# Kernel tuning notes

Measured on AMD Instinct MI355X. Metric: run time of the kernel, lower is better.

## Reference

```python
import jax, jax.numpy as jnp
import numpy as np

N_HEAD = 16
ROPE_BASE = 10000.0
ROPE_SCALE = 1.0

B, T, C = 4, 2048, 1024


def _rope_cos_sin(seq_len, head_dim, dtype):
    inv_freq = 1.0 / (ROPE_BASE ** (jnp.arange(0, head_dim, 2, dtype=jnp.float32) / head_dim))
    t = jnp.arange(seq_len, dtype=jnp.float32) * ROPE_SCALE
    freqs = jnp.einsum('t,d->td', t, inv_freq)          # [T, D/2]
    emb = jnp.concatenate([freqs, freqs], axis=-1)       # [T, D]
    return jnp.cos(emb).astype(dtype), jnp.sin(emb).astype(dtype)


def _rotate_half(x):
    x1, x2 = jnp.split(x, 2, axis=-1)
    return jnp.concatenate([-x2, x1], axis=-1)


def setup_inputs() -> dict:
    key = jax.random.key(0)
    ks = jax.random.split(key, 5)
    s = 1.0 / np.sqrt(C)  # modest init scale to keep logits sane
    return {
        'x': jax.random.normal(ks[0], (B, T, C), dtype=jnp.float32),
        'wq': jax.random.normal(ks[1], (C, C), dtype=jnp.float32) * s,
        'wk': jax.random.normal(ks[2], (C, C), dtype=jnp.float32) * s,
        'wv': jax.random.normal(ks[3], (C, C), dtype=jnp.float32) * s,
        'wp': jax.random.normal(ks[4], (C, C), dtype=jnp.float32) * s,
    }


def reference(x, wq, wk, wv, wp):
    # x: [B, T, C]; weights are torch Linear layout [out, in] -> y = x @ W.T
    Bx, Tx, Cx = x.shape
    H = N_HEAD
    D = Cx // H
    scale = D ** -0.5

    def split_heads(y):  # [B,T,C] -> [B,H,T,D]
        return y.reshape(Bx, Tx, H, D).transpose(0, 2, 1, 3)

    q = split_heads(x @ wq.T)
    k = split_heads(x @ wk.T)
    v = split_heads(x @ wv.T)

    cos, sin = _rope_cos_sin(Tx, D, x.dtype)  # [T, D] each
    cos = cos[None, None, :, :]
    sin = sin[None, None, :, :]
    q = q * cos + _rotate_half(q) * sin
    k = k * cos + _rotate_half(k) * sin

    att = jnp.einsum('bhtd,bhsd->bhts', q, k) * scale  # [B,H,T,T]
    causal = jnp.tril(jnp.ones((Tx, Tx), dtype=bool))
    att = jnp.where(causal[None, None], att, -jnp.inf)
    att = jax.nn.softmax(att, axis=-1)

    y = jnp.einsum('bhts,bhsd->bhtd', att, v)          # [B,H,T,D]
    y = y.transpose(0, 2, 1, 3).reshape(Bx, Tx, Cx)    # [B,T,C]
    return y @ wp.T
```

## Files before the change

kernel.cpp:

```cpp
#include <hip/hip_runtime.h>
#include <hip/hip_bf16.h>

typedef __attribute__((ext_vector_type(8))) short short8;
typedef __attribute__((ext_vector_type(4))) float f32x4;
typedef unsigned short u16;

#define DEV static __device__ __forceinline__

constexpr int Bsz = 4, Tn = 2048, Cn = 1024, Hn = 16, Dn = 64;
constexpr int TP = Tn + 32;
constexpr int VROWS = 64;
#define QSCL 0.1803368801111204f

DEV u16 f2bf(float f) {
    union { float f; unsigned u; } v{f};
    return (u16)((v.u + 0x8000u) >> 16);
}
DEV float bf2f(u16 u) {
    union { unsigned u; float f; } v;
    v.u = ((unsigned)u) << 16;
    return v.f;
}

DEV void gload_lds16(const void* g, void* l) {
    __builtin_amdgcn_global_load_lds((const __attribute__((address_space(1))) void*)g,
                                     (__attribute__((address_space(3))) void*)l, 16, 0, 0);
}

__global__ void cvt_kernel(const float* __restrict__ in, u16* __restrict__ out, int n4) {
    int i = blockIdx.x * blockDim.x + threadIdx.x;
    int stride = gridDim.x * blockDim.x;
    for (; i < n4; i += stride) {
        float4 v = ((const float4*)in)[i];
        short4 o;
        o.x = (short)f2bf(v.x); o.y = (short)f2bf(v.y);
        o.z = (short)f2bf(v.z); o.w = (short)f2bf(v.w);
        ((short4*)out)[i] = o;
    }
}

__global__ void cvtw_kernel(const float* __restrict__ w0, const float* __restrict__ w1,
                            const float* __restrict__ w2, const float* __restrict__ w3,
                            u16* o0, u16* o1, u16* o2, u16* o3) {
    const float* src = blockIdx.y == 0 ? w0 : blockIdx.y == 1 ? w1 : blockIdx.y == 2 ? w2 : w3;
    u16* dst = blockIdx.y == 0 ? o0 : blockIdx.y == 1 ? o1 : blockIdx.y == 2 ? o2 : o3;
    int i = blockIdx.x * blockDim.x + threadIdx.x;
    float4 v = ((const float4*)src)[i];
    short4 o;
    o.x = (short)f2bf(v.x); o.y = (short)f2bf(v.y);
    o.z = (short)f2bf(v.z); o.w = (short)f2bf(v.w);
    ((short4*)dst)[i] = o;
}

__global__ void trig_kernel(float* __restrict__ cs, float* __restrict__ sn) {
    int idx = blockIdx.x * blockDim.x + threadIdx.x;
    int t = idx >> 5, i = idx & 31;
    double inv = pow(10000.0, -(double)i / 32.0);
    double a = (double)t * inv;
    cs[idx] = (float)cos(a);
    sn[idx] = (float)sin(a);
}

template <int MODE>
__global__ __launch_bounds__(256, 2) void gemm_bt(
    const u16* __restrict__ A,
    const u16* __restrict__ B0, const u16* __restrict__ B1,
    void* __restrict__ O0, void* __restrict__ O1,
    const float* __restrict__ CS, const float* __restrict__ SN,
    int M, int N, int K) {
    __shared__ u16 As[128 * 32];
    __shared__ u16 Bs[128 * 32];

    const u16* Bp = B0;
    void* Op = O0;
    float scl = 1.0f;
    if (MODE == 0) {
        if (blockIdx.z == 1) { Bp = B1; Op = O1; }
        else scl = QSCL;
    }
    int tid = threadIdx.x;
    int w = tid >> 6, lane = tid & 63;
    int lr = lane & 15, lg = lane >> 4;
    int wr = w >> 1, wc = w & 1;
    long brow = (long)blockIdx.x * 128, bcol = (long)blockIdx.y * 128;

    f32x4 acc[4][4] = {};
    const u16* Arow = A + brow * K;
    const u16* Brow = Bp + bcol * K;

    for (int k0 = 0; k0 < K; k0 += 32) {
        __syncthreads();
#pragma unroll
        for (int c = 0; c < 2; c++) {
            int idx = c * 256 + tid;
            int row = idx >> 2, col = (idx & 3) << 3;
            const u16* ga = Arow + (long)row * K + k0 + col;
            const u16* gb = Brow + (long)row * K + k0 + col;
            char* la = (char*)As + (size_t)(c * 256 + (tid & 192)) * 16;
            char* lb = (char*)Bs + (size_t)(c * 256 + (tid & 192)) * 16;
            gload_lds16(ga, la);
            gload_lds16(gb, lb);
        }
        __syncthreads();
        short8 a[4], b[4];
#pragma unroll
        for (int i = 0; i < 4; i++)
            a[i] = *(const short8*)&As[(64 * wr + 16 * i + lr) * 32 + lg * 8];
#pragma unroll
        for (int j = 0; j < 4; j++)
            b[j] = *(const short8*)&Bs[(64 * wc + 16 * j + lr) * 32 + lg * 8];
#pragma unroll
        for (int i = 0; i < 4; i++)
#pragma unroll
            for (int j = 0; j < 4; j++)
                acc[i][j] = __builtin_amdgcn_mfma_f32_16x16x32_bf16(a[i], b[j], acc[i][j], 0, 0, 0);
    }

    if (MODE == 0) {
        u16* Op16 = (u16*)Op;
#pragma unroll
        for (int i = 0; i < 4; i++)
#pragma unroll
            for (int jj = 0; jj < 4; jj++) {
                long gr = brow + 64 * wr + 16 * i + lg * 4 + jj;
                long b_ = gr >> 11, t_ = gr & 2047;
#pragma unroll
                for (int j = 0; j < 2; j++) {
                    int di = 16 * j + lr;
                    float c = CS[(t_ << 5) + di], s = SN[(t_ << 5) + di];
                    float x1 = acc[i][j][jj], x2 = acc[i][j + 2][jj];
                    float o1 = (x1 * c - x2 * s) * scl;
                    float o2 = (x2 * c + x1 * s) * scl;
                    long gc = bcol + 64 * wc + 16 * j + lr;
                    long h_ = gc >> 6;
                    long base = (((b_ * Hn + h_) * Tn + t_) << 6) + (gc & 63);
                    Op16[base] = f2bf(o1);
                    Op16[base + 32] = f2bf(o2);
                }
            }
    } else {
#pragma unroll
        for (int i = 0; i < 4; i++)
#pragma unroll
            for (int j = 0; j < 4; j++)
#pragma unroll
                for (int jj = 0; jj < 4; jj++) {
                    long gr = brow + 64 * wr + 16 * i + lg * 4 + jj;
                    long gc = bcol + 64 * wc + 16 * j + lr;
                    float v = acc[i][j][jj];
                    if (MODE == 1) {
                        ((float*)Op)[gr * N + gc] = v;
                    } else {
                        long h_ = gr >> 6, d_ = gr & 63, b_ = gc >> 11, t_ = gc & 2047;
                        ((u16*)Op)[((b_ * Hn + h_) * VROWS + d_) * TP + t_] = f2bf(v);
                    }
                }
    }
}

__global__ __launch_bounds__(256, 2) void attn_kernel(
    const u16* __restrict__ Q, const u16* __restrict__ K, const u16* __restrict__ VT,
    u16* __restrict__ Yb) {
    __shared__ u16 plds[4][32][68];

    int tid = threadIdx.x;
    int w = tid >> 6, lane = tid & 63;
    int lr = lane & 15, lg = lane >> 4;
    int gid = blockIdx.x;
    int xcd = gid & 7;
    int sl = gid >> 3;
    int bh = ((sl >> 4) << 3) + xcd;
    int qt = 63 - ((sl & 15) * 4 + w);
    int q0 = qt * 32;

    const u16* Qp = Q + (long)bh * Tn * Dn;
    const u16* Kp = K + (long)bh * Tn * Dn;
    const u16* VTp = VT + (long)bh * VROWS * TP;
    long b_ = bh >> 4, h_ = bh & 15;

    short8 onesf;
#pragma unroll
    for (int j = 0; j < 8; j++) onesf[j] = (lr == 0) ? (short)0x3f80 : (short)0;

    short8 aq[2][2];
#pragma unroll
    for (int qi = 0; qi < 2; qi++)
#pragma unroll
        for (int ks = 0; ks < 2; ks++)
            aq[qi][ks] = *(const short8*)&Qp[(long)(q0 + qi * 16 + lr) * 64 + ks * 32 + lg * 8];

    f32x4 acc[2][5] = {};
    float m_[2][4];
#pragma unroll
    for (int qi = 0; qi < 2; qi++)
#pragma unroll
        for (int jj = 0; jj < 4; jj++) m_[qi][jj] = -1e30f;

    short8 bkc[4][2];
    auto load_bk = [&](short8 dst[4][2], int kv0) {
#pragma unroll
        for (int cblk = 0; cblk < 4; cblk++) {
            const u16* kb = &Kp[(long)(kv0 + cblk * 16 + lr) * 64 + lg * 8];
            dst[cblk][0] = *(const short8*)kb;
            dst[cblk][1] = *(const short8*)(kb + 32);
        }
    };
    load_bk(bkc, 0);

    auto iter = [&](auto mc, auto pfc, int kv0) {
        constexpr bool MASKED = decltype(mc)::value;
        constexpr bool PF = decltype(pfc)::value;
        short8 bv[2][4];
#pragma unroll
        for (int ks = 0; ks < 2; ks++)
#pragma unroll
            for (int dblk = 0; dblk < 4; dblk++)
                bv[ks][dblk] = *(const short8*)&VTp[(long)(dblk * 16 + lr) * TP + kv0 + ks * 32 + lg * 8];
        short8 bkn[4][2];
        if (PF) load_bk(bkn, kv0 + 64);
        f32x4 s[2][4];
#pragma unroll
        for (int cblk = 0; cblk < 4; cblk++)
#pragma unroll
            for (int qi = 0; qi < 2; qi++) {
                f32x4 sc = {};
                sc = __builtin_amdgcn_mfma_f32_16x16x32_bf16(aq[qi][0], bkc[cblk][0], sc, 0, 0, 0);
                sc = __builtin_amdgcn_mfma_f32_16x16x32_bf16(aq[qi][1], bkc[cblk][1], sc, 0, 0, 0);
                if (MASKED) {
                    int col = kv0 + cblk * 16 + lr;
#pragma unroll
                    for (int jj = 0; jj < 4; jj++) {
                        int row = q0 + qi * 16 + lg * 4 + jj;
                        if (col > row) sc[jj] = -1e30f;
                    }
                }
                s[qi][cblk] = sc;
            }
        float pm[2][4];
        bool grow = false;
#pragma unroll
        for (int qi = 0; qi < 2; qi++)
#pragma unroll
            for (int jj = 0; jj < 4; jj++) {
                pm[qi][jj] = fmaxf(fmaxf(s[qi][0][jj], s[qi][1][jj]),
                                   fmaxf(s[qi][2][jj], s[qi][3][jj]));
                grow = grow || (pm[qi][jj] > m_[qi][jj] + 8.0f);
            }
        if (__any(grow)) {
#pragma unroll
            for (int qi = 0; qi < 2; qi++)
#pragma unroll
                for (int jj = 0; jj < 4; jj++) {
                    float v = pm[qi][jj];
                    v = fmaxf(v, __shfl_xor(v, 1));
                    v = fmaxf(v, __shfl_xor(v, 2));
                    v = fmaxf(v, __shfl_xor(v, 4));
                    v = fmaxf(v, __shfl_xor(v, 8));
                    float mn = fmaxf(m_[qi][jj], v);
                    float alpha = __builtin_amdgcn_exp2f(m_[qi][jj] - mn);
                    m_[qi][jj] = mn;
#pragma unroll
                    for (int dblk = 0; dblk < 5; dblk++) acc[qi][dblk][jj] *= alpha;
                }
        }
#pragma unroll
        for (int qi = 0; qi < 2; qi++)
#pragma unroll
            for (int cblk = 0; cblk < 4; cblk++)
#pragma unroll
                for (int jj = 0; jj < 4; jj++)
                    plds[w][qi * 16 + lg * 4 + jj][cblk * 16 + lr] =
                        f2bf(__builtin_amdgcn_exp2f(s[qi][cblk][jj] - m_[qi][jj]));
        short8 pa[2][2];
#pragma unroll
        for (int qi = 0; qi < 2; qi++)
#pragma unroll
            for (int ks = 0; ks < 2; ks++)
                pa[qi][ks] = *(const short8*)&plds[w][qi * 16 + lr][ks * 32 + lg * 8];
#pragma unroll
        for (int ks = 0; ks < 2; ks++) {
#pragma unroll
            for (int dblk = 0; dblk < 4; dblk++)
#pragma unroll
                for (int qi = 0; qi < 2; qi++)
                    acc[qi][dblk] = __builtin_amdgcn_mfma_f32_16x16x32_bf16(
                        pa[qi][ks], bv[ks][dblk], acc[qi][dblk], 0, 0, 0);
#pragma unroll
            for (int qi = 0; qi < 2; qi++)
                acc[qi][4] = __builtin_amdgcn_mfma_f32_16x16x32_bf16(
                    pa[qi][ks], onesf, acc[qi][4], 0, 0, 0);
        }
        if (PF)
#pragma unroll
            for (int cblk = 0; cblk < 4; cblk++)
#pragma unroll
                for (int ks = 0; ks < 2; ks++)
                    bkc[cblk][ks] = bkn[cblk][ks];
    };

    int kv_end = q0 + 32;
    int last = ((kv_end - 1) >> 6) << 6;
    for (int kv0 = 0; kv0 < last; kv0 += 64)
        iter(std::integral_constant<bool, false>{}, std::integral_constant<bool, true>{}, kv0);
    iter(std::integral_constant<bool, true>{}, std::integral_constant<bool, false>{}, last);

#pragma unroll
    for (int qi = 0; qi < 2; qi++)
#pragma unroll
        for (int jj = 0; jj < 4; jj++) {
            float l = __shfl(acc[qi][4][jj], lane & 48);
            float rl = 1.0f / l;
            int row = q0 + qi * 16 + lg * 4 + jj;
#pragma unroll
            for (int dblk = 0; dblk < 4; dblk++) {
                int d = dblk * 16 + lr;
                Yb[((b_ * Tn + row) * Cn) + h_ * 64 + d] = f2bf(acc[qi][dblk][jj] * rl);
            }
        }
}

extern "C" void kernel_launch(void* const* d_in, const int* in_sizes, int n_in,
                              void* d_out, int out_size, void* d_ws, size_t ws_size,
                              hipStream_t stream) {
    const float* x  = (const float*)d_in[0];
    const float* wq = (const float*)d_in[1];
    const float* wk = (const float*)d_in[2];
    const float* wv = (const float*)d_in[3];
    const float* wp = (const float*)d_in[4];

    char* ws = (char*)d_ws;
    size_t off = 0;
    auto alloc = [&](size_t bytes) {
        char* p = ws + off;
        off += (bytes + 255) & ~(size_t)255;
        return p;
    };
    const size_t BTC = (size_t)Bsz * Tn * Cn;
    u16* xb  = (u16*)alloc(BTC * 2);
    u16* wqb = (u16*)alloc((size_t)Cn * Cn * 2);
    u16* wkb = (u16*)alloc((size_t)Cn * Cn * 2);
    u16* wvb = (u16*)alloc((size_t)Cn * Cn * 2);
    u16* wpb = (u16*)alloc((size_t)Cn * Cn * 2);
    u16* qr  = (u16*)alloc(BTC * 2);
    u16* kr  = (u16*)alloc(BTC * 2);
    u16* vt  = (u16*)alloc((size_t)64 * VROWS * TP * 2);
    float* cs = (float*)alloc((size_t)Tn * 32 * 4);
    float* sn = (float*)alloc((size_t)Tn * 32 * 4);
    u16* yb  = xb;

    int M = Bsz * Tn;
    cvt_kernel<<<1024, 256, 0, stream>>>(x, xb, (int)(BTC / 4));
    cvtw_kernel<<<dim3(Cn * Cn / 4 / 256, 4), 256, 0, stream>>>(
        wq, wk, wv, wp, wqb, wkb, wvb, wpb);
    trig_kernel<<<(Tn * 32) / 256, 256, 0, stream>>>(cs, sn);

    gemm_bt<0><<<dim3(M / 128, Cn / 128, 2), 256, 0, stream>>>(
        xb, wqb, wkb, qr, kr, cs, sn, M, Cn, Cn);

    gemm_bt<2><<<dim3(Cn / 128, M / 128), 256, 0, stream>>>(
        wvb, xb, nullptr, vt, nullptr, nullptr, nullptr, Cn, M, Cn);

    attn_kernel<<<dim3(1024), 256, 0, stream>>>(qr, kr, vt, yb);

    gemm_bt<1><<<dim3(M / 128, Cn / 128), 256, 0, stream>>>(
        yb, wpb, nullptr, d_out, nullptr, nullptr, nullptr, M, Cn, Cn);
}
```

Before: 248.1 us.

## Share K/V tiles across waves via double-buffered LDS staging

The attention kernel now assigns four contiguous 32-row query tiles to each block. It stages each 64-key K and V^T tile once into a swizzled, double-buffered LDS region using direct global-to-LDS loads, instead of every wave loading K and V from global memory into registers. This cuts redundant global/L2 traffic and register pressure, and the launch bound is raised to 3 blocks per CU. The cost is a block-wide barrier every iteration, idle waves on the diagonal tiles, and more LDS per block.

```diff
diff --git a/kernel.cpp b/kernel.cpp
--- a/kernel.cpp
+++ b/kernel.cpp
@@ -158,9 +158,10 @@
     }
 }
 
-__global__ __launch_bounds__(256, 2) void attn_kernel(
+__global__ __launch_bounds__(256, 3) void attn_kernel(
     const u16* __restrict__ Q, const u16* __restrict__ K, const u16* __restrict__ VT,
     u16* __restrict__ Yb) {
+    __shared__ char kvb[2][16384];
     __shared__ u16 plds[4][32][68];
 
     int tid = threadIdx.x;
@@ -170,8 +171,9 @@
     int xcd = gid & 7;
     int sl = gid >> 3;
     int bh = ((sl >> 4) << 3) + xcd;
-    int qt = 63 - ((sl & 15) * 4 + w);
-    int q0 = qt * 32;
+    int g = 15 - (sl & 15);
+    int qb0 = g * 128;
+    int q0 = qb0 + w * 32;
 
     const u16* Qp = Q + (long)bh * Tn * Dn;
     const u16* Kp = K + (long)bh * Tn * Dn;
@@ -196,113 +198,110 @@
 #pragma unroll
         for (int jj = 0; jj < 4; jj++) m_[qi][jj] = -1e30f;
 
-    short8 bkc[4][2];
-    auto load_bk = [&](short8 dst[4][2], int kv0) {
-#pragma unroll
-        for (int cblk = 0; cblk < 4; cblk++) {
-            const u16* kb = &Kp[(long)(kv0 + cblk * 16 + lr) * 64 + lg * 8];
-            dst[cblk][0] = *(const short8*)kb;
-            dst[cblk][1] = *(const short8*)(kb + 32);
+    int sub = lane >> 3;
+    int swz = ((lane & 7) ^ sub) << 3;
+    auto stage = [&](int buf, int kv0) {
+#pragma unroll
+        for (int k2 = 0; k2 < 2; k2++) {
+            int c = w * 2 + k2;
+            int r = c * 8 + sub;
+            gload_lds16(Kp + (long)(kv0 + r) * 64 + swz, kvb[buf] + c * 1024);
+            gload_lds16(VTp + (long)r * TP + kv0 + swz, kvb[buf] + 8192 + c * 1024);
         }
     };
-    load_bk(bkc, 0);
-
-    auto iter = [&](auto mc, auto pfc, int kv0) {
-        constexpr bool MASKED = decltype(mc)::value;
-        constexpr bool PF = decltype(pfc)::value;
-        short8 bv[2][4];
-#pragma unroll
-        for (int ks = 0; ks < 2; ks++)
-#pragma unroll
-            for (int dblk = 0; dblk < 4; dblk++)
-                bv[ks][dblk] = *(const short8*)&VTp[(long)(dblk * 16 + lr) * TP + kv0 + ks * 32 + lg * 8];
-        short8 bkn[4][2];
-        if (PF) load_bk(bkn, kv0 + 64);
-        f32x4 s[2][4];
-#pragma unroll
-        for (int cblk = 0; cblk < 4; cblk++)
-#pragma unroll
-            for (int qi = 0; qi < 2; qi++) {
-                f32x4 sc = {};
-                sc = __builtin_amdgcn_mfma_f32_16x16x32_bf16(aq[qi][0], bkc[cblk][0], sc, 0, 0, 0);
-                sc = __builtin_amdgcn_mfma_f32_16x16x32_bf16(aq[qi][1], bkc[cblk][1], sc, 0, 0, 0);
-                if (MASKED) {
-                    int col = kv0 + cblk * 16 + lr;
+
+    int nit = (qb0 + 128) >> 6;
+    stage(0, 0);
+
+    for (int it = 0; it < nit; ++it) {
+        int kv0 = it << 6;
+        __syncthreads();
+        if (it + 1 < nit) stage((it + 1) & 1, kv0 + 64);
+        if (kv0 < q0 + 32) {
+            const char* kb = kvb[it & 1];
+            f32x4 s[2][4];
+            bool masked = (kv0 + 63 > q0);
+#pragma unroll
+            for (int cblk = 0; cblk < 4; cblk++) {
+                int r = cblk * 16 + lr;
+                short8 bk0 = *(const short8*)(kb + r * 128 + ((lg * 16) ^ ((lr & 7) << 4)));
+                short8 bk1 = *(const short8*)(kb + r * 128 + ((64 + lg * 16) ^ ((lr & 7) << 4)));
+#pragma unroll
+                for (int qi = 0; qi < 2; qi++) {
+                    f32x4 sc = {};
+                    sc = __builtin_amdgcn_mfma_f32_16x16x32_bf16(aq[qi][0], bk0, sc, 0, 0, 0);
+                    sc = __builtin_amdgcn_mfma_f32_16x16x32_bf16(aq[qi][1], bk1, sc, 0, 0, 0);
+                    if (masked) {
+                        int col = kv0 + cblk * 16 + lr;
+#pragma unroll
+                        for (int jj = 0; jj < 4; jj++) {
+                            int row = q0 + qi * 16 + lg * 4 + jj;
+                            if (col > row) sc[jj] = -1e30f;
+                        }
+                    }
+                    s[qi][cblk] = sc;
+                }
+            }
+            float pm[2][4];
+            bool grow = false;
+#pragma unroll
+            for (int qi = 0; qi < 2; qi++)
+#pragma unroll
+                for (int jj = 0; jj < 4; jj++) {
+                    pm[qi][jj] = fmaxf(fmaxf(s[qi][0][jj], s[qi][1][jj]),
+                                       fmaxf(s[qi][2][jj], s[qi][3][jj]));
+                    grow = grow || (pm[qi][jj] > m_[qi][jj] + 8.0f);
+                }
+            if (__any(grow)) {
+#pragma unroll
+                for (int qi = 0; qi < 2; qi++)
 #pragma unroll
                     for (int jj = 0; jj < 4; jj++) {
-                        int row = q0 + qi * 16 + lg * 4 + jj;
-                        if (col > row) sc[jj] = -1e30f;
+                        float v = pm[qi][jj];
+                        v = fmaxf(v, __shfl_xor(v, 1));
+                        v = fmaxf(v, __shfl_xor(v, 2));
+                        v = fmaxf(v, __shfl_xor(v, 4));
+                        v = fmaxf(v, __shfl_xor(v, 8));
+                        float mn = fmaxf(m_[qi][jj], v);
+                        float alpha = __builtin_amdgcn_exp2f(m_[qi][jj] - mn);
+                        m_[qi][jj] = mn;
+#pragma unroll
+                        for (int dblk = 0; dblk < 5; dblk++) acc[qi][dblk][jj] *= alpha;
                     }
-                }
-                s[qi][cblk] = sc;
-            }
-        float pm[2][4];
-        bool grow = false;
-#pragma unroll
-        for (int qi = 0; qi < 2; qi++)
-#pragma unroll
-            for (int jj = 0; jj < 4; jj++) {
-                pm[qi][jj] = fmaxf(fmaxf(s[qi][0][jj], s[qi][1][jj]),
-                                   fmaxf(s[qi][2][jj], s[qi][3][jj]));
-                grow = grow || (pm[qi][jj] > m_[qi][jj] + 8.0f);
-            }
-        if (__any(grow)) {
+            }
 #pragma unroll
             for (int qi = 0; qi < 2; qi++)
 #pragma unroll
-                for (int jj = 0; jj < 4; jj++) {
-                    float v = pm[qi][jj];
-                    v = fmaxf(v, __shfl_xor(v, 1));
-                    v = fmaxf(v, __shfl_xor(v, 2));
-                    v = fmaxf(v, __shfl_xor(v, 4));
-                    v = fmaxf(v, __shfl_xor(v, 8));
-                    float mn = fmaxf(m_[qi][jj], v);
-                    float alpha = __builtin_amdgcn_exp2f(m_[qi][jj] - mn);
-                    m_[qi][jj] = mn;
-#pragma unroll
-                    for (int dblk = 0; dblk < 5; dblk++) acc[qi][dblk][jj] *= alpha;
-                }
+                for (int cblk = 0; cblk < 4; cblk++)
+#pragma unroll
+                    for (int jj = 0; jj < 4; jj++)
+                        plds[w][qi * 16 + lg * 4 + jj][cblk * 16 + lr] =
+                            f2bf(__builtin_amdgcn_exp2f(s[qi][cblk][jj] - m_[qi][jj]));
+            short8 pa[2][2];
+#pragma unroll
+            for (int qi = 0; qi < 2; qi++)
+#pragma unroll
+                for (int ks = 0; ks < 2; ks++)
+                    pa[qi][ks] = *(const short8*)&plds[w][qi * 16 + lr][ks * 32 + lg * 8];
+#pragma unroll
+            for (int ks = 0; ks < 2; ks++) {
+#pragma unroll
+                for (int dblk = 0; dblk < 4; dblk++) {
+                    int d = dblk * 16 + lr;
+                    short8 bv = *(const short8*)(kb + 8192 + d * 128 +
+                                                 ((ks * 64 + lg * 16) ^ ((lr & 7) << 4)));
+#pragma unroll
+                    for (int qi = 0; qi < 2; qi++)
+                        acc[qi][dblk] = __builtin_amdgcn_mfma_f32_16x16x32_bf16(
+                            pa[qi][ks], bv, acc[qi][dblk], 0, 0, 0);
+                }
+#pragma unroll
+                for (int qi = 0; qi < 2; qi++)
+                    acc[qi][4] = __builtin_amdgcn_mfma_f32_16x16x32_bf16(
+                        pa[qi][ks], onesf, acc[qi][4], 0, 0, 0);
+            }
         }
-#pragma unroll
-        for (int qi = 0; qi < 2; qi++)
-#pragma unroll
-            for (int cblk = 0; cblk < 4; cblk++)
-#pragma unroll
-                for (int jj = 0; jj < 4; jj++)
-                    plds[w][qi * 16 + lg * 4 + jj][cblk * 16 + lr] =
-                        f2bf(__builtin_amdgcn_exp2f(s[qi][cblk][jj] - m_[qi][jj]));
-        short8 pa[2][2];
-#pragma unroll
-        for (int qi = 0; qi < 2; qi++)
-#pragma unroll
-            for (int ks = 0; ks < 2; ks++)
-                pa[qi][ks] = *(const short8*)&plds[w][qi * 16 + lr][ks * 32 + lg * 8];
-#pragma unroll
-        for (int ks = 0; ks < 2; ks++) {
-#pragma unroll
-            for (int dblk = 0; dblk < 4; dblk++)
-#pragma unroll
-                for (int qi = 0; qi < 2; qi++)
-                    acc[qi][dblk] = __builtin_amdgcn_mfma_f32_16x16x32_bf16(
-                        pa[qi][ks], bv[ks][dblk], acc[qi][dblk], 0, 0, 0);
-#pragma unroll
-            for (int qi = 0; qi < 2; qi++)
-                acc[qi][4] = __builtin_amdgcn_mfma_f32_16x16x32_bf16(
-                    pa[qi][ks], onesf, acc[qi][4], 0, 0, 0);
-        }
-        if (PF)
-#pragma unroll
-            for (int cblk = 0; cblk < 4; cblk++)
-#pragma unroll
-                for (int ks = 0; ks < 2; ks++)
-                    bkc[cblk][ks] = bkn[cblk][ks];
-    };
-
-    int kv_end = q0 + 32;
-    int last = ((kv_end - 1) >> 6) << 6;
-    for (int kv0 = 0; kv0 < last; kv0 += 64)
-        iter(std::integral_constant<bool, false>{}, std::integral_constant<bool, true>{}, kv0);
-    iter(std::integral_constant<bool, true>{}, std::integral_constant<bool, false>{}, last);
+    }
 
 #pragma unroll
     for (int qi = 0; qi < 2; qi++)
```

Result: faster. 212.8 us (-14.2%).
